# Kernel tuning notes

Hardware: AMD Instinct MI355X
Metric: run time of the kernel (lower is better)

The kernel has to match this reference:

```python
import jax, jax.numpy as jnp
import numpy as np

N = 2048       # num_nodes
B = 32         # batch
UNITS = 64     # rnn_units
OUT_DIM = 1
K = 2          # max_diffusion_step


def _rw(a):
    # random-walk matrix D^-1 A
    d = a.sum(axis=1, keepdims=True)
    return a / jnp.maximum(d, 1e-8)


def _supports(adj):
    # dual_random_walk: forward and backward random-walk transitions (transposed, as in DCRNN)
    return [_rw(adj).T, _rw(adj.T).T]


def _gconv(supports, x_bnf, w, b):
    # x_bnf: (B, N, F). Faithful to DCRNN: x0 columns are F-major then B,
    # and x0/x1 are rebound across supports exactly like the original loop.
    B_, N_, F_ = x_bnf.shape
    x0 = x_bnf.transpose(1, 2, 0).reshape(N_, F_ * B_)
    xs = [x0]
    for S in supports:
        x1 = S @ x0
        xs.append(x1)
        for _ in range(2, K + 1):
            x2 = 2.0 * (S @ x1) - x0
            xs.append(x2)
            x1, x0 = x2, x1
    M = len(xs)  # num_supports*K + 1 = 5
    x = jnp.stack(xs).reshape(M, N_, F_, B_).transpose(3, 1, 2, 0).reshape(B_ * N_, F_ * M)
    return x @ w + b


def _cell(supports, inp_flat, hx_flat, wg, bg, wc, bc):
    B_ = inp_flat.shape[0]
    inp = inp_flat.reshape(B_, N, -1)
    hx = hx_flat.reshape(B_, N, UNITS)
    cat = jnp.concatenate([inp, hx], axis=-1)
    val = jax.nn.sigmoid(_gconv(supports, cat, wg, bg)).reshape(B_, N, 2 * UNITS)
    r, u = val[..., :UNITS], val[..., UNITS:]
    c = jnp.tanh(_gconv(supports, jnp.concatenate([inp, r * hx], axis=-1), wc, bc).reshape(B_, N, UNITS))
    h = u * hx + (1.0 - u) * c
    return h.reshape(B_, N * UNITS)


def setup_inputs() -> dict:
    key = jax.random.key(0)
    ks = jax.random.split(key, 10)
    s = 0.02
    return {
        "inputs": jax.random.normal(ks[0], (B, N * OUT_DIM), jnp.float32),
        "hidden_state": jax.random.normal(ks[1], (2, B, N * UNITS), jnp.float32),
        "adj_mx": jax.random.uniform(ks[2], (N, N), jnp.float32),
        "w_gate_0": jax.random.normal(ks[3], ((1 + UNITS) * 5, 2 * UNITS), jnp.float32) * s,
        "b_gate_0": jnp.ones((2 * UNITS,), jnp.float32),
        "w_cand_0": jax.random.normal(ks[4], ((1 + UNITS) * 5, UNITS), jnp.float32) * s,
        "b_cand_0": jnp.zeros((UNITS,), jnp.float32),
        "w_gate_1": jax.random.normal(ks[5], ((UNITS + UNITS) * 5, 2 * UNITS), jnp.float32) * s,
        "b_gate_1": jnp.ones((2 * UNITS,), jnp.float32),
        "w_cand_1": jax.random.normal(ks[6], ((UNITS + UNITS) * 5, UNITS), jnp.float32) * s,
        "b_cand_1": jnp.zeros((UNITS,), jnp.float32),
        "w_proj": jax.random.normal(ks[7], (UNITS, OUT_DIM), jnp.float32) * s,
        "b_proj": jnp.zeros((OUT_DIM,), jnp.float32),
    }


def reference(inputs, hidden_state, adj_mx, w_gate_0, b_gate_0, w_cand_0, b_cand_0,
              w_gate_1, b_gate_1, w_cand_1, b_cand_1, w_proj, b_proj):
    supports = _supports(adj_mx)
    h0 = _cell(supports, inputs, hidden_state[0], w_gate_0, b_gate_0, w_cand_0, b_cand_0)
    h1 = _cell(supports, h0, hidden_state[1], w_gate_1, b_gate_1, w_cand_1, b_cand_1)
    out = (h1.reshape(-1, UNITS) @ w_proj + b_proj).reshape(-1, N * OUT_DIM)
    return out, jnp.stack([h0, h1])
```

## Files before the change

kernel.cpp:

```cpp
#include <hip/hip_runtime.h>

typedef unsigned short u16;
typedef unsigned char u8;
typedef unsigned int u32;
typedef float f32x4 __attribute__((ext_vector_type(4)));
typedef __bf16 bf16x8 __attribute__((ext_vector_type(8)));
typedef int i32x8 __attribute__((ext_vector_type(8)));

#define SCL_A 0x77777777u
#define SCL_B1 0x7F7F7F7Fu
#define SCL_B256 0x77777777u

__device__ __forceinline__ u16 f2bf(float f){
  u32 u = __builtin_bit_cast(u32, f);
  u32 r = (u + 0x7fffu + ((u >> 16) & 1u)) >> 16;
  return (u16)r;
}
__device__ __forceinline__ float bf2f(u16 h){
  return __builtin_bit_cast(float, ((u32)h) << 16);
}
__device__ __forceinline__ u8 f2e4(float x){
  return (u8)(__builtin_amdgcn_cvt_pk_fp8_f32(x, x, 0, false) & 0xff);
}
__device__ __forceinline__ u32 pack4_e4(float a, float b, float c, float d){
  int w = __builtin_amdgcn_cvt_pk_fp8_f32(a, b, 0, false);
  w = __builtin_amdgcn_cvt_pk_fp8_f32(c, d, w, true);
  return (u32)w;
}
__device__ __forceinline__ void gl_lds16(const void* g, void* l){
  __builtin_amdgcn_global_load_lds((__attribute__((address_space(1))) void*)g,
                                   (__attribute__((address_space(3))) void*)l,
                                   16, 0, 0);
}
__device__ __forceinline__ float sigf(float x){ return 1.f/(1.f + __expf(-x)); }

__device__ __forceinline__ void xcd_swizzle(int& x, int& y, int& z){
  int gx = gridDim.x, gy = gridDim.y;
  int nwg = gx * gy * gridDim.z;
  int lid = blockIdx.x + gx*(blockIdx.y + gy*blockIdx.z);
  int cpx = nwg >> 3;
  int swz = (lid & 7)*cpx + (lid >> 3);
  x = swz % gx;
  int rest = swz / gx;
  y = rest % gy;
  z = rest / gy;
}

__global__ __launch_bounds__(256) void k_rowsum(const float* __restrict__ adj, float* __restrict__ inv_rs,
                                                float* __restrict__ cs){
  int j = blockIdx.x; int tid = threadIdx.x;
  float s = 0.f;
  for (int i = tid; i < 2048; i += 256) s += adj[(long)j*2048 + i];
  for (int off = 32; off; off >>= 1) s += __shfl_down(s, off, 64);
  __shared__ float red[4];
  if ((tid & 63) == 0) red[tid >> 6] = s;
  __syncthreads();
  if (tid == 0){
    float t = red[0] + red[1] + red[2] + red[3];
    inv_rs[j] = 1.f / fmaxf(t, 1e-8f);
    cs[j] = 0.f;
  }
}

__global__ __launch_bounds__(256) void k_colsum2(const float* __restrict__ adj, float* __restrict__ cs){
  int j0 = blockIdx.x * 64, i0 = blockIdx.y * 128;
  int jj = threadIdx.x & 63, w = threadIdx.x >> 6;
  float s = 0.f;
  for (int i = w; i < 128; i += 4) s += adj[(long)(i0+i)*2048 + j0 + jj];
  __shared__ float red[256];
  red[threadIdx.x] = s;
  __syncthreads();
  if (w == 0){
    float t = red[jj] + red[64+jj] + red[128+jj] + red[192+jj];
    atomicAdd(&cs[j0+jj], t);
  }
}

__global__ __launch_bounds__(256) void k_build_S(const float* __restrict__ adj,
                                                 const float* __restrict__ inv_rs,
                                                 const float* __restrict__ cs,
                                                 u16* __restrict__ S0, u8* __restrict__ S0q,
                                                 u8* __restrict__ S0Tq, u8* __restrict__ S1q){
  __shared__ float t[64*66];
  __shared__ float rsl[64];
  __shared__ float icl[64];
  int i0 = blockIdx.x * 64, j0 = blockIdx.y * 64;
  int tid = threadIdx.x;
  if (tid < 64) rsl[tid] = inv_rs[j0 + tid];
  else if (tid >= 64 && tid < 128) icl[tid-64] = 1.f / fmaxf(cs[i0 + tid-64], 1e-8f);
  __syncthreads();
  for (int e = tid; e < 4096; e += 256){
    int jj = e >> 6, ii = e & 63;
    float a = adj[(long)(j0+jj)*2048 + i0 + ii];
    t[jj*66 + ii] = a;
    long o = (long)(j0+jj)*2048 + i0 + ii;
    S0Tq[o] = f2e4(a * rsl[jj] * 256.f);
    S1q[o]  = f2e4(a * icl[ii] * 256.f);
  }
  __syncthreads();
  for (int e = tid; e < 4096; e += 256){
    int ii = e >> 6, jj = e & 63;
    u16 vb = f2bf(t[jj*66 + ii] * rsl[jj]);
    long o = (long)(i0+ii)*2048 + j0 + jj;
    S0[o] = vb;
    S0q[o] = f2e4(bf2f(vb)*256.f);
  }
}

__global__ __launch_bounds__(256) void k_packW4(const float* __restrict__ wg0, const float* __restrict__ wc0,
                                                const float* __restrict__ wg1, const float* __restrict__ wc1,
                                                u16* __restrict__ WTg0, u16* __restrict__ WTc0,
                                                u16* __restrict__ WTg1, u16* __restrict__ WTc1){
  int z = blockIdx.y;
  const float* w = (z==0) ? wg0 : (z==1) ? wc0 : (z==2) ? wg1 : wc1;
  u16* WT       = (z==0) ? WTg0 : (z==1) ? WTc0 : (z==2) ? WTg1 : WTc1;
  int OUTr = (z==0 || z==2) ? 128 : 64;
  int F  = (z < 2) ? 65 : 128;
  int Fp = (z < 2) ? 72 : 128;
  int Kd = (z < 2) ? 384 : 640;
  int idx = blockIdx.x*256 + threadIdx.x;
  if (idx >= 128*Kd) return;
  int o = idx / Kd, k = idx - o*Kd;
  int m = k / Fp, f = k - m*Fp;
  float v = 0.f;
  if (o < OUTr && m < 5 && f < F) v = w[(long)(f*5 + m)*OUTr + o];
  WT[idx] = f2bf(v);
}

__global__ __launch_bounds__(256) void k_hx_build(const float* __restrict__ hx, const float* __restrict__ inp,
                                                  u8* __restrict__ X0T, u16* __restrict__ D,
                                                  int Fp, int rowoff, long ldD, int coloff, int l0extras){
  __shared__ float t[64*66];
  int b = blockIdx.x, n0 = blockIdx.y * 64;
  int tid = threadIdx.x;
  const float* hb = hx + (long)b*2048*64;
  long bn0 = (long)b*2048 + n0;
  for (int e = tid; e < 4096; e += 256){
    int u = e & 63, ni = e >> 6;
    t[ni*66 + u] = hb[(long)(n0+ni)*64 + u];
  }
  __syncthreads();
  for (int e = tid; e < 4096; e += 256){
    int u = e >> 6, ni = e & 63;
    X0T[((long)b*Fp + rowoff + u)*2048 + n0 + ni] = f2e4(t[ni*66 + u]);
  }
  for (int e = tid; e < 4096; e += 256){
    int ni = e >> 6, u = e & 63;
    D[(bn0 + ni)*ldD + coloff + u] = f2bf(t[ni*66 + u]);
  }
  if (l0extras){
    if (tid < 64){
      float v = inp[(long)b*2048 + n0 + tid];
      X0T[((long)b*Fp)*2048 + n0 + tid] = f2e4(v);
      D[(bn0 + tid)*ldD] = f2bf(v);
    }
    for (int e = tid; e < 7*64; e += 256){
      int f = 65 + (e >> 6), ni = e & 63;
      X0T[((long)b*Fp + f)*2048 + n0 + ni] = 0;
    }
    for (int e = tid; e < 64*31; e += 256){
      int ni = e / 31, wc = e - ni*31;
      int col = (wc < 7) ? (65 + wc) : (353 + wc);
      D[(bn0 + ni)*ldD + col] = 0;
    }
  }
}

__device__ __forceinline__ void gemm_core(const u16* __restrict__ A, const u16* __restrict__ Bt,
                                          int K, long tM, long tC,
                                          u16* lA, u16* lB, f32x4 (&acc)[4][4]){
  int tid = threadIdx.x;
  int wv = tid >> 6, lane = tid & 63;
  int q = lane >> 4, r16 = lane & 15;

  const u16* ga[4]; const u16* gb[4];
  u16* la[4]; u16* lb[4];
  #pragma unroll
  for (int it = 0; it < 4; it++){
    int L = it*256 + tid;
    int r = L >> 3, g = (L & 7) ^ (r & 7);
    ga[it] = A  + (tM + r)*(long)K + g*8;
    gb[it] = Bt + (tC + r)*(long)K + g*8;
    la[it] = lA + (it*256 + wv*64)*8;
    lb[it] = lB + (it*256 + wv*64)*8;
  }

  #pragma unroll
  for (int i = 0; i < 4; i++)
    #pragma unroll
    for (int j = 0; j < 4; j++){ acc[i][j][0]=0.f; acc[i][j][1]=0.f; acc[i][j][2]=0.f; acc[i][j][3]=0.f; }

  int wm = wv & 1, wn = wv >> 1;
  int aoff[4][2], boff[4][2];
  #pragma unroll
  for (int s = 0; s < 4; s++){
    int m = wm*64 + s*16 + r16;
    int n = wn*64 + s*16 + r16;
    #pragma unroll
    for (int h = 0; h < 2; h++){
      aoff[s][h] = (m*8 + ((h*4 + q) ^ (m & 7))) * 8;
      boff[s][h] = (n*8 + ((h*4 + q) ^ (n & 7))) * 8;
    }
  }

  for (int k0 = 0; k0 < K; k0 += 64){
    __syncthreads();
    #pragma unroll
    for (int it = 0; it < 4; it++){
      gl_lds16(ga[it] + k0, la[it]);
      gl_lds16(gb[it] + k0, lb[it]);
    }
    asm volatile("s_waitcnt vmcnt(0)" ::: "memory");
    __syncthreads();
    #pragma unroll
    for (int h = 0; h < 2; h++){
      bf16x8 af[4], bfr[4];
      #pragma unroll
      for (int s = 0; s < 4; s++){
        af[s]  = *(const bf16x8*)&lA[aoff[s][h]];
        bfr[s] = *(const bf16x8*)&lB[boff[s][h]];
      }
      #pragma unroll
      for (int i = 0; i < 4; i++)
        #pragma unroll
        for (int j = 0; j < 4; j++)
          acc[i][j] = __builtin_amdgcn_mfma_f32_16x16x32_bf16(af[i], bfr[j], acc[i][j], 0, 0, 0);
    }
  }
}

template<u32 SCLB>
__device__ __forceinline__ void gemm_core8(const u8* __restrict__ A, const u8* __restrict__ Bt,
                                           int K, long tM, long tC,
                                           u8* lA, u8* lB, f32x4 (&acc)[4][4]){
  int tid = threadIdx.x;
  int wv = tid >> 6, lane = tid & 63;
  int q = lane >> 4, r16 = lane & 15;

  const u8* ga[4]; const u8* gb[4];
  u8* la[4]; u8* lb[4];
  #pragma unroll
  for (int it = 0; it < 4; it++){
    int L = it*256 + tid;
    int r = L >> 3, x = (L & 7) ^ (r & 7);
    int g = ((x & 3) << 1) | (x >> 2);
    ga[it] = A  + (tM + r)*(long)K + g*16;
    gb[it] = Bt + (tC + r)*(long)K + g*16;
    la[it] = lA + (it*256 + wv*64)*16;
    lb[it] = lB + (it*256 + wv*64)*16;
  }

  #pragma unroll
  for (int i = 0; i < 4; i++)
    #pragma unroll
    for (int j = 0; j < 4; j++){ acc[i][j][0]=0.f; acc[i][j][1]=0.f; acc[i][j][2]=0.f; acc[i][j][3]=0.f; }

  int wm = wv & 1, wn = wv >> 1;
  int aoff[4][2], boff[4][2];
  #pragma unroll
  for (int s = 0; s < 4; s++){
    int m = wm*64 + s*16 + r16;
    int n = wn*64 + s*16 + r16;
    #pragma unroll
    for (int e = 0; e < 2; e++){
      aoff[s][e] = m*128 + ((e*4 + q) ^ (m & 7)) * 16;
      boff[s][e] = n*128 + ((e*4 + q) ^ (n & 7)) * 16;
    }
  }

  for (int k0 = 0; k0 < K; k0 += 128){
    __syncthreads();
    #pragma unroll
    for (int it = 0; it < 4; it++){
      gl_lds16(ga[it] + k0, la[it]);
      gl_lds16(gb[it] + k0, lb[it]);
    }
    asm volatile("s_waitcnt vmcnt(0)" ::: "memory");
    __syncthreads();
    i32x8 af[4];
    #pragma unroll
    for (int s = 0; s < 4; s++){
      uint4 a0 = *(const uint4*)&lA[aoff[s][0]];
      uint4 a1 = *(const uint4*)&lA[aoff[s][1]];
      i32x8 av; av[0]=a0.x; av[1]=a0.y; av[2]=a0.z; av[3]=a0.w; av[4]=a1.x; av[5]=a1.y; av[6]=a1.z; av[7]=a1.w;
      af[s] = av;
    }
    #pragma unroll
    for (int j = 0; j < 4; j++){
      uint4 b0 = *(const uint4*)&lB[boff[j][0]];
      uint4 b1 = *(const uint4*)&lB[boff[j][1]];
      i32x8 bv; bv[0]=b0.x; bv[1]=b0.y; bv[2]=b0.z; bv[3]=b0.w; bv[4]=b1.x; bv[5]=b1.y; bv[6]=b1.z; bv[7]=b1.w;
      #pragma unroll
      for (int i = 0; i < 4; i++)
        acc[i][j] = __builtin_amdgcn_mfma_scale_f32_16x16x128_f8f6f4(
                      af[i], bv, acc[i][j], 0, 0, 0, SCL_A, 0, SCLB);
    }
  }
}

__global__ __launch_bounds__(256, 4) void gemm_pre8(const u8* __restrict__ S0Tq, const u8* __restrict__ S1q,
                                                    const u8* __restrict__ S0q,
                                                    u8* __restrict__ Rq, u8* __restrict__ RTq, u8* __restrict__ Vq){
  __shared__ u8 lA[16384];
  __shared__ u8 lB[16384];
  f32x4 acc[4][4];
  int bx, by, bz;
  xcd_swizzle(bx, by, bz);
  const u8* Bt = (bz == 0) ? S1q : S0q;
  long tM = (long)bx * 128, tC = (long)by * 128;
  gemm_core8<SCL_B256>(S0Tq, Bt, 2048, tM, tC, lA, lB, acc);

  int tid = threadIdx.x, wv = tid >> 6, lane = tid & 63;
  int q = lane >> 4, r16 = lane & 15, wm = wv & 1, wn = wv >> 1;
  #pragma unroll
  for (int i = 0; i < 4; i++){
    long gi = tM + wm*64 + i*16 + q*4;
    #pragma unroll
    for (int j = 0; j < 4; j++){
      long gc = tC + wn*64 + j*16 + r16;
      f32x4 v = acc[i][j];
      if (bz == 0){
        *(u32*)(Rq + gc*2048 + gi) = pack4_e4(v[0]*256.f, v[1]*256.f, v[2]*256.f, v[3]*256.f);
        RTq[(gi+0)*2048 + gc] = f2e4(v[0]*256.f);
        RTq[(gi+1)*2048 + gc] = f2e4(v[1]*256.f);
        RTq[(gi+2)*2048 + gc] = f2e4(v[2]*256.f);
        RTq[(gi+3)*2048 + gc] = f2e4(v[3]*256.f);
      } else {
        float x0 = 2.f*v[0] - ((gi+0) == gc ? 1.f : 0.f);
        float x1 = 2.f*v[1] - ((gi+1) == gc ? 1.f : 0.f);
        float x2 = 2.f*v[2] - ((gi+2) == gc ? 1.f : 0.f);
        float x3 = 2.f*v[3] - ((gi+3) == gc ? 1.f : 0.f);
        *(u32*)(Vq + gc*2048 + gi) = pack4_e4(x0*256.f, x1*256.f, x2*256.f, x3*256.f);
      }
    }
  }
}

__global__ __launch_bounds__(256, 4) void gemm_w8(const u8* __restrict__ RTq, const u8* __restrict__ S1q,
                                                  const u16* __restrict__ S0, u8* __restrict__ Wq){
  __shared__ u8 lA[16384];
  __shared__ u8 lB[16384];
  f32x4 acc[4][4];
  int bx, by, bz;
  xcd_swizzle(bx, by, bz);
  long tM = (long)bx * 128, tC = (long)by * 128;
  gemm_core8<SCL_B256>(RTq, S1q, 2048, tM, tC, lA, lB, acc);

  int tid = threadIdx.x, wv = tid >> 6, lane = tid & 63;
  int q = lane >> 4, r16 = lane & 15, wm = wv & 1, wn = wv >> 1;
  #pragma unroll
  for (int i = 0; i < 4; i++){
    long gi = tM + wm*64 + i*16 + q*4;
    #pragma unroll
    for (int j = 0; j < 4; j++){
      long gc = tC + wn*64 + j*16 + r16;
      f32x4 v = acc[i][j];
      ushort4 x0 = *(const ushort4*)(S0 + gc*2048 + gi);
      *(u32*)(Wq + gc*2048 + gi) = pack4_e4((2.f*v[0] - bf2f(x0.x))*256.f,
                                            (2.f*v[1] - bf2f(x0.y))*256.f,
                                            (2.f*v[2] - bf2f(x0.z))*256.f,
                                            (2.f*v[3] - bf2f(x0.w))*256.f);
    }
  }
}

template<int FP>
__global__ __launch_bounds__(256, 4) void gemm_diff8(const u8* __restrict__ M0, const u8* __restrict__ M1,
                                                     const u8* __restrict__ M2, const u8* __restrict__ M3,
                                                     const u8* __restrict__ X, u16* __restrict__ D, long ldD){
  __shared__ u8 lA[16384];
  __shared__ u8 lB[16384];
  f32x4 acc[4][4];
  int bx, by, z;
  xcd_swizzle(bx, by, z);
  const u8* A = (z == 0) ? M0 : (z == 1) ? M1 : (z == 2) ? M2 : M3;
  long tM = (long)bx * 128, tC = (long)by * 128;
  gemm_core8<SCL_B1>(A, X, 2048, tM, tC, lA, lB, acc);

  int tid = threadIdx.x, wv = tid >> 6, lane = tid & 63;
  int q = lane >> 4, r16 = lane & 15, wm = wv & 1, wn = wv >> 1;
  int zb = (z + 1) * FP;
  #pragma unroll
  for (int i = 0; i < 4; i++){
    long gi = tM + wm*64 + i*16 + q*4;
    #pragma unroll
    for (int j = 0; j < 4; j++){
      int gc = (int)(tC + wn*64 + j*16 + r16);
      int b = gc / FP, f = gc - b*FP;
      long rb = (long)b*2048 + gi;
      f32x4 v = acc[i][j];
      D[(rb+0)*ldD + zb + f] = f2bf(v[0]);
      D[(rb+1)*ldD + zb + f] = f2bf(v[1]);
      D[(rb+2)*ldD + zb + f] = f2bf(v[2]);
      D[(rb+3)*ldD + zb + f] = f2bf(v[3]);
    }
  }
}

__global__ __launch_bounds__(256, 4) void gemm_diff8_c(const u8* __restrict__ M0, const u8* __restrict__ M1,
                                                       const u8* __restrict__ M2, const u8* __restrict__ M3,
                                                       const u8* __restrict__ Xr, u16* __restrict__ D,
                                                       long ldD, int Fp, int fin){
  __shared__ u8 lA[16384];
  __shared__ u8 lB[16384];
  f32x4 acc[4][4];
  int bx, by, z;
  xcd_swizzle(bx, by, z);
  const u8* A = (z == 0) ? M0 : (z == 1) ? M1 : (z == 2) ? M2 : M3;
  long tM = (long)bx * 128, tC = (long)by * 128;
  gemm_core8<SCL_B1>(A, Xr, 2048, tM, tC, lA, lB, acc);

  int tid = threadIdx.x, wv = tid >> 6, lane = tid & 63;
  int q = lane >> 4, r16 = lane & 15, wm = wv & 1, wn = wv >> 1;
  int zb = (z + 1) * Fp + fin;
  #pragma unroll
  for (int i = 0; i < 4; i++){
    long gi = tM + wm*64 + i*16 + q*4;
    #pragma unroll
    for (int j = 0; j < 4; j++){
      int gc = (int)(tC + wn*64 + j*16 + r16);
      int b = gc >> 6, u = gc & 63;
      long rb = (long)b*2048 + gi;
      f32x4 v = acc[i][j];
      D[(rb+0)*ldD + zb + u] = f2bf(v[0]);
      D[(rb+1)*ldD + zb + u] = f2bf(v[1]);
      D[(rb+2)*ldD + zb + u] = f2bf(v[2]);
      D[(rb+3)*ldD + zb + u] = f2bf(v[3]);
    }
  }
}

__global__ __launch_bounds__(256) void gemm_dense(const u16* __restrict__ A, const u16* __restrict__ Bt,
                                                  u16* __restrict__ Out, int K, long ldOut){
  __shared__ u16 lA[8192];
  __shared__ u16 lB[8192];
  f32x4 acc[4][4];
  long tM = (long)blockIdx.x * 128, tC = (long)blockIdx.y * 128;
  gemm_core(A, Bt, K, tM, tC, lA, lB, acc);

  int tid = threadIdx.x, wv = tid >> 6, lane = tid & 63;
  int q = lane >> 4, r16 = lane & 15, wm = wv & 1, wn = wv >> 1;
  #pragma unroll
  for (int i = 0; i < 4; i++){
    long gi = tM + wm*64 + i*16 + q*4;
    #pragma unroll
    for (int j = 0; j < 4; j++){
      long gc = tC + wn*64 + j*16 + r16;
      f32x4 v = acc[i][j];
      ushort4 o;
      o.x = f2bf(v[0]); o.y = f2bf(v[1]); o.z = f2bf(v[2]); o.w = f2bf(v[3]);
      *(ushort4*)(Out + gc*ldOut + gi) = o;
    }
  }
}

__global__ __launch_bounds__(256) void k_gate_ep(const u16* __restrict__ GT, const float* __restrict__ bg,
                                                 const float* __restrict__ hid, u8* __restrict__ Xr8,
                                                 u16* __restrict__ D, long ldD, int coloff){
  __shared__ float t[64*66];
  __shared__ u16 tb[64*66];
  int b = blockIdx.x, n0 = blockIdx.y * 64;
  int tid = threadIdx.x;
  long bn0 = (long)b*2048 + n0;
  for (int e = tid; e < 4096; e += 256){
    int u = e & 63, ni = e >> 6;
    t[ni*66 + u] = hid[(bn0 + ni)*64 + u];
  }
  __syncthreads();
  for (int e = tid; e < 4096; e += 256){
    int u = e >> 6, ni = e & 63;
    float r = sigf(bf2f(GT[(long)u*65536 + bn0 + ni]) + bg[u]);
    float pv = r * t[ni*66 + u];
    Xr8[((long)b*64 + u)*2048 + n0 + ni] = f2e4(pv);
    tb[ni*66 + u] = f2bf(pv);
  }
  __syncthreads();
  for (int e = tid; e < 4096; e += 256){
    int ni = e >> 6, u = e & 63;
    D[(bn0 + ni)*ldD + coloff + u] = tb[ni*66 + u];
  }
}

__global__ __launch_bounds__(256) void k_cand_ep(const u16* __restrict__ CT, const u16* __restrict__ GT,
                                                 const float* __restrict__ bc, const float* __restrict__ bg,
                                                 const float* __restrict__ hx, float* __restrict__ hout,
                                                 u8* __restrict__ X0T_next, u16* __restrict__ Dnext,
                                                 const float* __restrict__ wproj, const float* __restrict__ bproj,
                                                 float* __restrict__ out){
  __shared__ u16 tc[64*66];
  __shared__ u16 tu[64*66];
  __shared__ u16 th[64*66];
  int b = blockIdx.x, n0 = blockIdx.y * 64;
  int tid = threadIdx.x;
  long bn0 = (long)b*2048 + n0;
  for (int e = tid; e < 4096; e += 256){
    int u = e >> 6, ni = e & 63;
    float cv = tanhf(bf2f(CT[(long)u*65536 + bn0 + ni]) + bc[u]);
    float uv = sigf(bf2f(GT[(long)(64+u)*65536 + bn0 + ni]) + bg[64+u]);
    tc[ni*66 + u] = f2bf(cv);
    tu[ni*66 + u] = f2bf(uv);
  }
  __syncthreads();
  int lane = tid & 63, wv = tid >> 6;
  for (int it = 0; it < 16; ++it){
    int ni = it*4 + wv, u = lane;
    float hxv = hx[(bn0 + ni)*64 + u];
    float uv = bf2f(tu[ni*66 + u]), cv = bf2f(tc[ni*66 + u]);
    float h = uv*hxv + (1.f - uv)*cv;
    hout[(bn0 + ni)*64 + u] = h;
    if (Dnext) Dnext[(bn0 + ni)*640 + u] = f2bf(h);
    th[ni*66 + u] = f2bf(h);
    if (wproj){
      float v = h * wproj[u];
      for (int off = 32; off; off >>= 1) v += __shfl_down(v, off, 64);
      if (lane == 0) out[(long)b*2048 + n0 + ni] = v + bproj[0];
    }
  }
  __syncthreads();
  if (X0T_next){
    for (int e = tid; e < 4096; e += 256){
      int u = e >> 6, ni = e & 63;
      X0T_next[((long)b*128 + u)*2048 + n0 + ni] = f2e4(bf2f(th[ni*66 + u]));
    }
  }
}

extern "C" void kernel_launch(void* const* d_in, const int* in_sizes, int n_in,
                              void* d_out, int out_size, void* d_ws, size_t ws_size,
                              hipStream_t stream){
  (void)in_sizes; (void)n_in; (void)out_size; (void)ws_size;
  const float* inputs = (const float*)d_in[0];
  const float* hidden = (const float*)d_in[1];
  const float* adj    = (const float*)d_in[2];
  const float* wg0 = (const float*)d_in[3];
  const float* bg0 = (const float*)d_in[4];
  const float* wc0 = (const float*)d_in[5];
  const float* bc0 = (const float*)d_in[6];
  const float* wg1 = (const float*)d_in[7];
  const float* bg1 = (const float*)d_in[8];
  const float* wc1 = (const float*)d_in[9];
  const float* bc1 = (const float*)d_in[10];
  const float* wp  = (const float*)d_in[11];
  const float* bp  = (const float*)d_in[12];
  float* out = (float*)d_out;

  char* p = (char*)d_ws;
  auto alloc = [&](size_t bytes)->char*{ char* r = p; p += (bytes + 255) & ~(size_t)255; return r; };
  float* inv_rs = (float*)alloc(2048*4);
  float* cs     = (float*)alloc(2048*4);
  const size_t SB  = (size_t)2048*2048*2;
  const size_t SB8 = (size_t)2048*2048;
  u16* S0  = (u16*)alloc(SB);
  u8*  S0q = (u8*)alloc(SB8);
  u8*  S0Tq= (u8*)alloc(SB8);
  u8*  S1q = (u8*)alloc(SB8);
  u8*  Rq  = (u8*)alloc(SB8);
  u8*  RTq = (u8*)alloc(SB8);
  u8*  Vq  = (u8*)alloc(SB8);
  u8*  Wq  = (u8*)alloc(SB8);
  u8*  X0a8 = (u8*)alloc((size_t)2304*2048);
  u8*  X0b8 = (u8*)alloc((size_t)4096*2048);
  u8*  Xr8  = (u8*)alloc(SB8);
  u16* D   = (u16*)alloc((size_t)65536*640*2);
  u16* GT = (u16*)alloc((size_t)128*65536*2);
  u16* CT = (u16*)alloc((size_t)128*65536*2);
  u16* WTg0 = (u16*)alloc((size_t)128*384*2);
  u16* WTc0 = (u16*)alloc((size_t)128*384*2);
  u16* WTg1 = (u16*)alloc((size_t)128*640*2);
  u16* WTc1 = (u16*)alloc((size_t)128*640*2);

  const float* hid0 = hidden;
  const float* hid1 = hidden + (size_t)4194304;
  float* h0out = out + 65536;
  float* h1out = out + 65536 + 4194304;

  k_rowsum<<<2048, 256, 0, stream>>>(adj, inv_rs, cs);
  k_colsum2<<<dim3(32,16), 256, 0, stream>>>(adj, cs);
  k_build_S<<<dim3(32,32), 256, 0, stream>>>(adj, inv_rs, cs, S0, S0q, S0Tq, S1q);
  k_packW4<<<dim3(320,4), 256, 0, stream>>>(wg0, wc0, wg1, wc1, WTg0, WTc0, WTg1, WTc1);
  k_hx_build<<<dim3(32,32), 256, 0, stream>>>(hid0, inputs, X0a8, D, 72, 1, 384, 1, 1);

  gemm_pre8<<<dim3(16,16,2), 256, 0, stream>>>(S0Tq, S1q, S0q, Rq, RTq, Vq);
  gemm_w8  <<<dim3(16,16),   256, 0, stream>>>(RTq, S1q, S0, Wq);

  dim3 gD0(16, 18, 4), gD1(16, 32, 4), gDc(16, 16, 4), gDen(512, 1), gE(32, 32);

  gemm_diff8<72><<<gD0, 256, 0, stream>>>(S0q, Vq, Rq, Wq, X0a8, D, 384);
  gemm_dense<<<gDen, 256, 0, stream>>>(D, WTg0, GT, 384, 65536);
  k_gate_ep<<<gE, 256, 0, stream>>>(GT, bg0, hid0, Xr8, D, 384, 1);

  gemm_diff8_c<<<gDc, 256, 0, stream>>>(S0q, Vq, Rq, Wq, Xr8, D, 384, 72, 1);
  gemm_dense<<<gDen, 256, 0, stream>>>(D, WTc0, CT, 384, 65536);
  k_cand_ep<<<gE, 256, 0, stream>>>(CT, GT, bc0, bg0, hid0, h0out, X0b8, D, nullptr, nullptr, nullptr);

  k_hx_build<<<dim3(32,32), 256, 0, stream>>>(hid1, nullptr, X0b8, D, 128, 64, 640, 64, 0);

  gemm_diff8<128><<<gD1, 256, 0, stream>>>(S0q, Vq, Rq, Wq, X0b8, D, 640);
  gemm_dense<<<gDen, 256, 0, stream>>>(D, WTg1, GT, 640, 65536);
  k_gate_ep<<<gE, 256, 0, stream>>>(GT, bg1, hid1, Xr8, D, 640, 64);

  gemm_diff8_c<<<gDc, 256, 0, stream>>>(S0q, Vq, Rq, Wq, Xr8, D, 640, 128, 64);
  gemm_dense<<<gDen, 256, 0, stream>>>(D, WTc1, CT, 640, 65536);
  k_cand_ep<<<gE, 256, 0, stream>>>(CT, GT, bc1, bg1, hid1, h1out, nullptr, nullptr, wp, bp, out);
}
```

Baseline: 531.4 us.

## Fuse gate and candidate epilogues into dense GEMM kernels

Merges the gate epilogue (sigmoid, reset-times-hidden, fp8/bf16 staging) and the candidate epilogue (tanh, GRU update, projection reduction) into the dense weight GEMM kernels. This removes the intermediate GT/CT round trips and four separate launches. It also splits the D buffer into per-layer D0/D1 so the layer-0 candidate can write the next layer's inputs directly. Only the update half of GT is still stored. The cost is more epilogue work and LDS staging in the GEMM kernels, plus uncoalesced strided hx and hout accesses in the epilogue.

```diff
diff --git a/kernel.cpp b/kernel.cpp
--- a/kernel.cpp
+++ b/kernel.cpp
@@ -430,97 +430,150 @@
   }
 }
 
-__global__ __launch_bounds__(256) void gemm_dense(const u16* __restrict__ A, const u16* __restrict__ Bt,
-                                                  u16* __restrict__ Out, int K, long ldOut){
-  __shared__ u16 lA[8192];
-  __shared__ u16 lB[8192];
+__global__ __launch_bounds__(256) void gemm_dense_gate(const u16* __restrict__ A, const u16* __restrict__ Bt,
+                                                       int K, const float* __restrict__ bg,
+                                                       const float* __restrict__ hx,
+                                                       u16* __restrict__ GT,
+                                                       u8* __restrict__ Xr8,
+                                                       u16* __restrict__ D, long ldD, int coloff){
+  __shared__ __align__(16) u8 smem[32768];
+  u16* lA = (u16*)smem;
+  u16* lB = (u16*)(smem + 16384);
   f32x4 acc[4][4];
-  long tM = (long)blockIdx.x * 128, tC = (long)blockIdx.y * 128;
-  gemm_core(A, Bt, K, tM, tC, lA, lB, acc);
+  long tM = (long)blockIdx.x * 128;
+  gemm_core(A, Bt, K, tM, 0, lA, lB, acc);
 
   int tid = threadIdx.x, wv = tid >> 6, lane = tid & 63;
   int q = lane >> 4, r16 = lane & 15, wm = wv & 1, wn = wv >> 1;
-  #pragma unroll
-  for (int i = 0; i < 4; i++){
-    long gi = tM + wm*64 + i*16 + q*4;
-    #pragma unroll
-    for (int j = 0; j < 4; j++){
-      long gc = tC + wn*64 + j*16 + r16;
-      f32x4 v = acc[i][j];
-      ushort4 o;
-      o.x = f2bf(v[0]); o.y = f2bf(v[1]); o.z = f2bf(v[2]); o.w = f2bf(v[3]);
-      *(ushort4*)(Out + gc*ldOut + gi) = o;
-    }
-  }
-}
-
-__global__ __launch_bounds__(256) void k_gate_ep(const u16* __restrict__ GT, const float* __restrict__ bg,
-                                                 const float* __restrict__ hid, u8* __restrict__ Xr8,
-                                                 u16* __restrict__ D, long ldD, int coloff){
-  __shared__ float t[64*66];
-  __shared__ u16 tb[64*66];
-  int b = blockIdx.x, n0 = blockIdx.y * 64;
-  int tid = threadIdx.x;
-  long bn0 = (long)b*2048 + n0;
-  for (int e = tid; e < 4096; e += 256){
-    int u = e & 63, ni = e >> 6;
-    t[ni*66 + u] = hid[(bn0 + ni)*64 + u];
-  }
-  __syncthreads();
-  for (int e = tid; e < 4096; e += 256){
-    int u = e >> 6, ni = e & 63;
-    float r = sigf(bf2f(GT[(long)u*65536 + bn0 + ni]) + bg[u]);
-    float pv = r * t[ni*66 + u];
-    Xr8[((long)b*64 + u)*2048 + n0 + ni] = f2e4(pv);
-    tb[ni*66 + u] = f2bf(pv);
-  }
-  __syncthreads();
-  for (int e = tid; e < 4096; e += 256){
-    int ni = e >> 6, u = e & 63;
-    D[(bn0 + ni)*ldD + coloff + u] = tb[ni*66 + u];
-  }
-}
-
-__global__ __launch_bounds__(256) void k_cand_ep(const u16* __restrict__ CT, const u16* __restrict__ GT,
-                                                 const float* __restrict__ bc, const float* __restrict__ bg,
-                                                 const float* __restrict__ hx, float* __restrict__ hout,
-                                                 u8* __restrict__ X0T_next, u16* __restrict__ Dnext,
-                                                 const float* __restrict__ wproj, const float* __restrict__ bproj,
-                                                 float* __restrict__ out){
-  __shared__ u16 tc[64*66];
-  __shared__ u16 tu[64*66];
-  __shared__ u16 th[64*66];
-  int b = blockIdx.x, n0 = blockIdx.y * 64;
-  int tid = threadIdx.x;
-  long bn0 = (long)b*2048 + n0;
-  for (int e = tid; e < 4096; e += 256){
-    int u = e >> 6, ni = e & 63;
-    float cv = tanhf(bf2f(CT[(long)u*65536 + bn0 + ni]) + bc[u]);
-    float uv = sigf(bf2f(GT[(long)(64+u)*65536 + bn0 + ni]) + bg[64+u]);
-    tc[ni*66 + u] = f2bf(cv);
-    tu[ni*66 + u] = f2bf(uv);
-  }
-  __syncthreads();
-  int lane = tid & 63, wv = tid >> 6;
-  for (int it = 0; it < 16; ++it){
-    int ni = it*4 + wv, u = lane;
-    float hxv = hx[(bn0 + ni)*64 + u];
-    float uv = bf2f(tu[ni*66 + u]), cv = bf2f(tc[ni*66 + u]);
-    float h = uv*hxv + (1.f - uv)*cv;
-    hout[(bn0 + ni)*64 + u] = h;
-    if (Dnext) Dnext[(bn0 + ni)*640 + u] = f2bf(h);
-    th[ni*66 + u] = f2bf(h);
-    if (wproj){
-      float v = h * wproj[u];
-      for (int off = 32; off; off >>= 1) v += __shfl_down(v, off, 64);
-      if (lane == 0) out[(long)b*2048 + n0 + ni] = v + bproj[0];
-    }
-  }
-  __syncthreads();
+  int b = (int)(tM >> 11), n0 = (int)(tM & 2047);
+  u16* stg16 = (u16*)smem;
+  u8*  stg8  = smem + 16896;
+
+  __syncthreads();
+  if (wn == 0){
+    #pragma unroll
+    for (int i = 0; i < 4; i++){
+      int tokb = wm*64 + i*16 + q*4;
+      long gtok = tM + tokb;
+      #pragma unroll
+      for (int j = 0; j < 4; j++){
+        int c = j*16 + r16;
+        float bgc = bg[c];
+        f32x4 v = acc[i][j];
+        float p0 = sigf(v[0] + bgc) * hx[(gtok+0)*64 + c];
+        float p1 = sigf(v[1] + bgc) * hx[(gtok+1)*64 + c];
+        float p2 = sigf(v[2] + bgc) * hx[(gtok+2)*64 + c];
+        float p3 = sigf(v[3] + bgc) * hx[(gtok+3)*64 + c];
+        stg16[(tokb+0)*66 + c] = f2bf(p0);
+        stg16[(tokb+1)*66 + c] = f2bf(p1);
+        stg16[(tokb+2)*66 + c] = f2bf(p2);
+        stg16[(tokb+3)*66 + c] = f2bf(p3);
+        *(u32*)&stg8[c*132 + tokb] = pack4_e4(p0, p1, p2, p3);
+      }
+    }
+  } else {
+    #pragma unroll
+    for (int i = 0; i < 4; i++){
+      long gi = tM + wm*64 + i*16 + q*4;
+      #pragma unroll
+      for (int j = 0; j < 4; j++){
+        int c = 64 + j*16 + r16;
+        float bgc = bg[c];
+        f32x4 v = acc[i][j];
+        ushort4 o;
+        o.x = f2bf(sigf(v[0] + bgc));
+        o.y = f2bf(sigf(v[1] + bgc));
+        o.z = f2bf(sigf(v[2] + bgc));
+        o.w = f2bf(sigf(v[3] + bgc));
+        *(ushort4*)(GT + (long)c*65536 + gi) = o;
+      }
+    }
+  }
+  __syncthreads();
+  for (int e = tid; e < 8192; e += 256){
+    int tok = e >> 6, c = e & 63;
+    D[(tM + tok)*ldD + coloff + c] = stg16[tok*66 + c];
+  }
+  for (int e = tid; e < 2048; e += 256){
+    int c = e >> 5, seg = e & 31;
+    *(u32*)(Xr8 + ((long)b*64 + c)*2048 + n0 + seg*4) = *(const u32*)&stg8[c*132 + seg*4];
+  }
+}
+
+__global__ __launch_bounds__(256) void gemm_dense_cand(const u16* __restrict__ A, const u16* __restrict__ Bt,
+                                                       int K, const float* __restrict__ bc,
+                                                       const u16* __restrict__ GT,
+                                                       const float* __restrict__ hx,
+                                                       float* __restrict__ hout,
+                                                       u8* __restrict__ X0T_next,
+                                                       u16* __restrict__ Dnext, long ldDn, int colDn,
+                                                       const float* __restrict__ wproj,
+                                                       const float* __restrict__ bproj,
+                                                       float* __restrict__ out){
+  __shared__ __align__(16) u8 smem[32768];
+  u16* lA = (u16*)smem;
+  u16* lB = (u16*)(smem + 16384);
+  f32x4 acc[4][4];
+  long tM = (long)blockIdx.x * 128;
+  gemm_core(A, Bt, K, tM, 0, lA, lB, acc);
+
+  int tid = threadIdx.x, wv = tid >> 6, lane = tid & 63;
+  int q = lane >> 4, r16 = lane & 15, wm = wv & 1, wn = wv >> 1;
+  int b = (int)(tM >> 11), n0 = (int)(tM & 2047);
+  u16* stg16 = (u16*)smem;
+
+  __syncthreads();
+  if (wn == 0){
+    #pragma unroll
+    for (int i = 0; i < 4; i++){
+      int tokb = wm*64 + i*16 + q*4;
+      long gtok = tM + tokb;
+      float psum0 = 0.f, psum1 = 0.f, psum2 = 0.f, psum3 = 0.f;
+      #pragma unroll
+      for (int j = 0; j < 4; j++){
+        int c = j*16 + r16;
+        float bcc = bc[c];
+        float wpc = wproj ? wproj[c] : 0.f;
+        f32x4 v = acc[i][j];
+        #pragma unroll
+        for (int rr = 0; rr < 4; rr++){
+          float cv = bf2f(f2bf(tanhf(v[rr] + bcc)));
+          float uv = bf2f(GT[(long)(64+c)*65536 + gtok + rr]);
+          float hxv = hx[(gtok+rr)*64 + c];
+          float h = uv*hxv + (1.f - uv)*cv;
+          hout[(gtok+rr)*64 + c] = h;
+          stg16[(tokb+rr)*66 + c] = f2bf(h);
+          float hw = h * wpc;
+          if (rr == 0) psum0 += hw; else if (rr == 1) psum1 += hw;
+          else if (rr == 2) psum2 += hw; else psum3 += hw;
+        }
+      }
+      if (wproj){
+        float ps[4] = {psum0, psum1, psum2, psum3};
+        #pragma unroll
+        for (int rr = 0; rr < 4; rr++){
+          float vv = ps[rr];
+          vv += __shfl_xor(vv, 1, 64);
+          vv += __shfl_xor(vv, 2, 64);
+          vv += __shfl_xor(vv, 4, 64);
+          vv += __shfl_xor(vv, 8, 64);
+          if (r16 == 0) out[gtok + rr] = vv + bproj[0];
+        }
+      }
+    }
+  }
+  __syncthreads();
+  if (Dnext){
+    for (int e = tid; e < 8192; e += 256){
+      int tok = e >> 6, c = e & 63;
+      Dnext[(tM + tok)*ldDn + colDn + c] = stg16[tok*66 + c];
+    }
+  }
   if (X0T_next){
-    for (int e = tid; e < 4096; e += 256){
-      int u = e >> 6, ni = e & 63;
-      X0T_next[((long)b*128 + u)*2048 + n0 + ni] = f2e4(bf2f(th[ni*66 + u]));
+    for (int e = tid; e < 8192; e += 256){
+      int c = e >> 7, tok = e & 127;
+      u16 hb = stg16[tok*66 + c];
+      X0T_next[((long)b*128 + c)*2048 + n0 + tok] = f2e4(bf2f(hb));
     }
   }
 }
@@ -561,9 +614,9 @@
   u8*  X0a8 = (u8*)alloc((size_t)2304*2048);
   u8*  X0b8 = (u8*)alloc((size_t)4096*2048);
   u8*  Xr8  = (u8*)alloc(SB8);
-  u16* D   = (u16*)alloc((size_t)65536*640*2);
+  u16* D0  = (u16*)alloc((size_t)65536*384*2);
+  u16* D1  = (u16*)alloc((size_t)65536*640*2);
   u16* GT = (u16*)alloc((size_t)128*65536*2);
-  u16* CT = (u16*)alloc((size_t)128*65536*2);
   u16* WTg0 = (u16*)alloc((size_t)128*384*2);
   u16* WTc0 = (u16*)alloc((size_t)128*384*2);
   u16* WTg1 = (u16*)alloc((size_t)128*640*2);
@@ -578,28 +631,26 @@
   k_colsum2<<<dim3(32,16), 256, 0, stream>>>(adj, cs);
   k_build_S<<<dim3(32,32), 256, 0, stream>>>(adj, inv_rs, cs, S0, S0q, S0Tq, S1q);
   k_packW4<<<dim3(320,4), 256, 0, stream>>>(wg0, wc0, wg1, wc1, WTg0, WTc0, WTg1, WTc1);
-  k_hx_build<<<dim3(32,32), 256, 0, stream>>>(hid0, inputs, X0a8, D, 72, 1, 384, 1, 1);
+  k_hx_build<<<dim3(32,32), 256, 0, stream>>>(hid0, inputs, X0a8, D0, 72, 1, 384, 1, 1);
 
   gemm_pre8<<<dim3(16,16,2), 256, 0, stream>>>(S0Tq, S1q, S0q, Rq, RTq, Vq);
   gemm_w8  <<<dim3(16,16),   256, 0, stream>>>(RTq, S1q, S0, Wq);
 
-  dim3 gD0(16, 18, 4), gD1(16, 32, 4), gDc(16, 16, 4), gDen(512, 1), gE(32, 32);
-
-  gemm_diff8<72><<<gD0, 256, 0, stream>>>(S0q, Vq, Rq, Wq, X0a8, D, 384);
-  gemm_dense<<<gDen, 256, 0, stream>>>(D, WTg0, GT, 384, 65536);
-  k_gate_ep<<<gE, 256, 0, stream>>>(GT, bg0, hid0, Xr8, D, 384, 1);
-
-  gemm_diff8_c<<<gDc, 256, 0, stream>>>(S0q, Vq, Rq, Wq, Xr8, D, 384, 72, 1);
-  gemm_dense<<<gDen, 256, 0, stream>>>(D, WTc0, CT, 384, 65536);
-  k_cand_ep<<<gE, 256, 0, stream>>>(CT, GT, bc0, bg0, hid0, h0out, X0b8, D, nullptr, nullptr, nullptr);
-
-  k_hx_build<<<dim3(32,32), 256, 0, stream>>>(hid1, nullptr, X0b8, D, 128, 64, 640, 64, 0);
-
-  gemm_diff8<128><<<gD1, 256, 0, stream>>>(S0q, Vq, Rq, Wq, X0b8, D, 640);
-  gemm_dense<<<gDen, 256, 0, stream>>>(D, WTg1, GT, 640, 65536);
-  k_gate_ep<<<gE, 256, 0, stream>>>(GT, bg1, hid1, Xr8, D, 640, 64);
-
-  gemm_diff8_c<<<gDc, 256, 0, stream>>>(S0q, Vq, Rq, Wq, Xr8, D, 640, 128, 64);
-  gemm_dense<<<gDen, 256, 0, stream>>>(D, WTc1, CT, 640, 65536);
-  k_cand_ep<<<gE, 256, 0, stream>>>(CT, GT, bc1, bg1, hid1, h1out, nullptr, nullptr, wp, bp, out);
-}
+  dim3 gD0(16, 18, 4), gD1(16, 32, 4), gDc(16, 16, 4), gDen(512, 1);
+
+  gemm_diff8<72><<<gD0, 256, 0, stream>>>(S0q, Vq, Rq, Wq, X0a8, D0, 384);
+  gemm_dense_gate<<<gDen, 256, 0, stream>>>(D0, WTg0, 384, bg0, hid0, GT, Xr8, D0, 384, 1);
+
+  gemm_diff8_c<<<gDc, 256, 0, stream>>>(S0q, Vq, Rq, Wq, Xr8, D0, 384, 72, 1);
+  gemm_dense_cand<<<gDen, 256, 0, stream>>>(D0, WTc0, 384, bc0, GT, hid0, h0out,
+                                            X0b8, D1, 640, 0, nullptr, nullptr, nullptr);
+
+  k_hx_build<<<dim3(32,32), 256, 0, stream>>>(hid1, nullptr, X0b8, D1, 128, 64, 640, 64, 0);
+
+  gemm_diff8<128><<<gD1, 256, 0, stream>>>(S0q, Vq, Rq, Wq, X0b8, D1, 640);
+  gemm_dense_gate<<<gDen, 256, 0, stream>>>(D1, WTg1, 640, bg1, hid1, GT, Xr8, D1, 640, 64);
+
+  gemm_diff8_c<<<gDc, 256, 0, stream>>>(S0q, Vq, Rq, Wq, Xr8, D1, 640, 128, 64);
+  gemm_dense_cand<<<gDen, 256, 0, stream>>>(D1, WTc1, 640, bc1, GT, hid1, h1out,
+                                            nullptr, nullptr, 0, 0, wp, bp, out);
+}
```

After: 570.6 us, median of 2. 1.07x slower.
